# Optimization experiments

Measured on AMD Instinct MI355X. Metric: run time of the kernel, lower is better.

Reference implementation:

```python
import jax, jax.numpy as jnp
import numpy as np

N0, N1, N2 = 200000, 50000, 10000   # source nodes, hop-1 targets, final targets
D, C, DEG = 256, 40, 10


def _sage(x_src, x_tgt, row, col, n_tgt, Wl, Wr, b, reduce):
    # PyG SAGEConv: lin_l(aggr(messages)) + lin_r(x_target); bias on lin_l only
    msg = x_src[row]                                   # [E, D] gather
    if reduce == 'mean':
        s = jax.ops.segment_sum(msg, col, num_segments=n_tgt)
        cnt = jax.ops.segment_sum(jnp.ones((row.shape[0], 1), msg.dtype), col, num_segments=n_tgt)
        agg = s / jnp.maximum(cnt, 1.0)
    else:
        agg = jax.ops.segment_max(msg, col, num_segments=n_tgt)
    return agg @ Wl + b + x_tgt @ Wr


def setup_inputs() -> dict:
    key = jax.random.key(0)
    ks = jax.random.split(key, 16)
    x = jax.random.normal(ks[0], (N0, D), jnp.float32)
    # every target gets exactly DEG sampled neighbors (NeighborSampler-style)
    row0 = jax.random.randint(ks[1], (N1 * DEG,), 0, N0, jnp.int32)
    col0 = jnp.repeat(jnp.arange(N1, dtype=jnp.int32), DEG)
    edge_index0 = jnp.stack([row0, col0])
    row1 = jax.random.randint(ks[2], (N2 * DEG,), 0, N1, jnp.int32)
    col1 = jnp.repeat(jnp.arange(N2, dtype=jnp.int32), DEG)
    edge_index1 = jnp.stack([row1, col1])
    s = 1.0 / np.sqrt(D)
    w = lambda k, shp: jax.random.uniform(k, shp, jnp.float32, -s, s)
    return {
        'x': x, 'edge_index0': edge_index0, 'edge_index1': edge_index1,
        'Wl_m0': w(ks[3], (D, D)), 'Wr_m0': w(ks[4], (D, D)), 'b_m0': jnp.zeros((D,), jnp.float32),
        'Wl_x0': w(ks[5], (D, D)), 'Wr_x0': w(ks[6], (D, D)), 'b_x0': jnp.zeros((D,), jnp.float32),
        'Wl_m1': w(ks[7], (D, D)), 'Wr_m1': w(ks[8], (D, D)), 'b_m1': jnp.zeros((D,), jnp.float32),
        'Wl_x1': w(ks[9], (D, D)), 'Wr_x1': w(ks[10], (D, D)), 'b_x1': jnp.zeros((D,), jnp.float32),
        'W_post': w(ks[11], (2 * D, C)), 'b_post': jnp.zeros((C,), jnp.float32),
    }


def reference(x, edge_index0, edge_index1,
              Wl_m0, Wr_m0, b_m0, Wl_x0, Wr_x0, b_x0,
              Wl_m1, Wr_m1, b_m1, Wl_x1, Wr_x1, b_x1,
              W_post, b_post):
    row0, col0 = edge_index0[0], edge_index0[1]
    row1, col1 = edge_index1[0], edge_index1[1]
    tgt0 = x[:N1]
    h_m = jax.nn.relu(_sage(x, tgt0, row0, col0, N1, Wl_m0, Wr_m0, b_m0, 'mean'))
    h_x = jax.nn.relu(_sage(x, tgt0, row0, col0, N1, Wl_x0, Wr_x0, b_x0, 'max'))
    # NOTE: faithful to source bug: layer-1 target features are the RAW x[:size[1]]
    tgt1 = x[:N2]
    o_m = _sage(h_m, tgt1, row1, col1, N2, Wl_m1, Wr_m1, b_m1, 'mean')
    o_x = _sage(h_x, tgt1, row1, col1, N2, Wl_x1, Wr_x1, b_x1, 'max')
    out = jnp.concatenate([o_m, o_x], axis=-1) @ W_post + b_post
    return jax.nn.log_softmax(out, axis=-1)
```

## Files before the change

kernel.cpp:

```cpp
#include <hip/hip_runtime.h>
#include <hip/hip_bf16.h>
#include <math.h>

#define N0v 200000
#define N1v 50000
#define N2v 10000
#define Dv  256
#define Cv  40
#define DEGv 10

typedef __attribute__((ext_vector_type(8))) short          s16x8;
typedef __attribute__((ext_vector_type(8))) unsigned short u16x8;
typedef __attribute__((ext_vector_type(4))) float          f32x4;

static __device__ __forceinline__ unsigned short f2bf(float f) {
    __hip_bfloat16 h = __float2bfloat16(f);
    return *reinterpret_cast<unsigned short*>(&h);
}
static __device__ __forceinline__ float bf2f(unsigned short u) {
    __hip_bfloat16 h = *reinterpret_cast<__hip_bfloat16*>(&u);
    return __bfloat162float(h);
}

static __device__ __forceinline__ void gload16(const void* g, void* l) {
    __builtin_amdgcn_global_load_lds(
        (const __attribute__((address_space(1))) unsigned int*)g,
        (__attribute__((address_space(3))) unsigned int*)l, 16, 0, 0);
}

__global__ __launch_bounds__(256) void prep_kernel(
    const float* __restrict__ x, unsigned short* __restrict__ xtb,
    const float* __restrict__ Wl0, const float* __restrict__ Wr0,
    const float* __restrict__ Wl1, const float* __restrict__ Wr1,
    const float* __restrict__ Wl2, const float* __restrict__ Wr2,
    const float* __restrict__ Wl3, const float* __restrict__ Wr3,
    unsigned short* __restrict__ WT0, unsigned short* __restrict__ WT1,
    unsigned short* __restrict__ WT2, unsigned short* __restrict__ WT3)
{
    const int b = blockIdx.x;
    const int tid = threadIdx.x;
    if (b < 6250) {
        const int i = (b * 256 + tid) * 8;
        float4 v0 = *(const float4*)(x + i);
        float4 v1 = *(const float4*)(x + i + 4);
        unsigned short o[8] = { f2bf(v0.x), f2bf(v0.y), f2bf(v0.z), f2bf(v0.w),
                                f2bf(v1.x), f2bf(v1.y), f2bf(v1.z), f2bf(v1.w) };
        *(u16x8*)(xtb + i) = *(u16x8*)o;
    } else {
        const int idx = b - 6250;
        const int p = idx >> 8;
        const int n = idx & 255;
        const float* Wl = (p == 0) ? Wl0 : (p == 1) ? Wl1 : (p == 2) ? Wl2 : Wl3;
        const float* Wr = (p == 0) ? Wr0 : (p == 1) ? Wr1 : (p == 2) ? Wr2 : Wr3;
        unsigned short* WT = (p == 0) ? WT0 : (p == 1) ? WT1 : (p == 2) ? WT2 : WT3;
        WT[(size_t)n * 512 + tid]       = f2bf(Wl[(size_t)tid * Dv + n]);
        WT[(size_t)n * 512 + 256 + tid] = f2bf(Wr[(size_t)tid * Dv + n]);
    }
}

__global__ __launch_bounds__(256) void agg0_kernel(
    const float* __restrict__ x, const int* __restrict__ row,
    unsigned short* __restrict__ om, unsigned short* __restrict__ ox)
{
    const int t = blockIdx.x * 4 + (threadIdx.x >> 6);
    const int c = threadIdx.x & 63;
    const int eb = t * DEGv;
    float4 s = make_float4(0.f, 0.f, 0.f, 0.f);
    float4 mx = make_float4(-INFINITY, -INFINITY, -INFINITY, -INFINITY);
#pragma unroll
    for (int k = 0; k < DEGv; ++k) {
        const int r = row[eb + k];
        float4 v = ((const float4*)x)[(size_t)r * 64 + c];
        s.x += v.x; s.y += v.y; s.z += v.z; s.w += v.w;
        mx.x = fmaxf(mx.x, v.x); mx.y = fmaxf(mx.y, v.y);
        mx.z = fmaxf(mx.z, v.z); mx.w = fmaxf(mx.w, v.w);
    }
    const float inv = 1.0f / DEGv;
    unsigned short osum[4] = { f2bf(s.x * inv), f2bf(s.y * inv), f2bf(s.z * inv), f2bf(s.w * inv) };
    unsigned short omax[4] = { f2bf(mx.x), f2bf(mx.y), f2bf(mx.z), f2bf(mx.w) };
    *(uint2*)&om[(size_t)t * Dv + c * 4] = *(uint2*)osum;
    *(uint2*)&ox[(size_t)t * Dv + c * 4] = *(uint2*)omax;
}

__global__ __launch_bounds__(256) void agg1_kernel(
    const unsigned short* __restrict__ hm, const unsigned short* __restrict__ hx,
    const int* __restrict__ row,
    unsigned short* __restrict__ om, unsigned short* __restrict__ ox)
{
    const int t = blockIdx.x * 8 + (threadIdx.x >> 5);
    const int c = threadIdx.x & 31;
    const int eb = t * DEGv;
    float s[8] = {};
    float mx[8] = { -INFINITY, -INFINITY, -INFINITY, -INFINITY,
                    -INFINITY, -INFINITY, -INFINITY, -INFINITY };
#pragma unroll
    for (int k = 0; k < DEGv; ++k) {
        const int r = row[eb + k];
        u16x8 vm = ((const u16x8*)hm)[(size_t)r * 32 + c];
        u16x8 vx = ((const u16x8*)hx)[(size_t)r * 32 + c];
#pragma unroll
        for (int j = 0; j < 8; ++j) {
            s[j]  += bf2f(vm[j]);
            mx[j]  = fmaxf(mx[j], bf2f(vx[j]));
        }
    }
    const float inv = 1.0f / DEGv;
    unsigned short osum[8], omax[8];
#pragma unroll
    for (int j = 0; j < 8; ++j) { osum[j] = f2bf(s[j] * inv); omax[j] = f2bf(mx[j]); }
    *(u16x8*)&om[(size_t)t * Dv + c * 8] = *(u16x8*)osum;
    *(u16x8*)&ox[(size_t)t * Dv + c * 8] = *(u16x8*)omax;
}

template<int RELU, int OUTBF>
__global__ __launch_bounds__(256) void gemm_mfma_kernel(
    const unsigned short* __restrict__ A1a, const unsigned short* __restrict__ A1b,
    const unsigned short* __restrict__ A2,
    const unsigned short* __restrict__ WTa, const unsigned short* __restrict__ WTb,
    const float* __restrict__ biasa, const float* __restrict__ biasb,
    void* outa, void* outb, int M, int ldc, int col_step)
{
    __shared__ unsigned short Asb[128 * 64];
    __shared__ unsigned short Bsb[128 * 64];

    const int z = blockIdx.z;
    const unsigned short* A1 = z ? A1b : A1a;
    const unsigned short* WT = z ? WTb : WTa;
    const float* bias = z ? biasb : biasa;
    void* outp = z ? outb : outa;
    const int col_off = z * col_step;

    const int tid  = threadIdx.x;
    const int lane = tid & 63;
    const int w    = tid >> 6;
    const int wr   = w >> 1, wc = w & 1;
    const int m0   = blockIdx.x * 128, n0 = blockIdx.y * 128;

    const int lrow = lane >> 3;
    const int scol = ((lane & 7) ^ lrow) * 8;

    const unsigned short* pA1[4];
    const unsigned short* pA2[4];
    const unsigned short* pB[4];
    unsigned short* lA[4];
    unsigned short* lB[4];
#pragma unroll
    for (int c = 0; c < 4; ++c) {
        const int r = w * 32 + c * 8 + lrow;
        int gm = m0 + r; if (gm >= M) gm = M - 1;
        pA1[c] = A1 + (size_t)gm * Dv + scol;
        pA2[c] = A2 + (size_t)gm * Dv + scol;
        pB[c]  = WT + (size_t)(n0 + r) * 512 + scol;
        lA[c] = &Asb[(w * 32 + c * 8) * 64];
        lB[c] = &Bsb[(w * 32 + c * 8) * 64];
    }

    const int fr = lane & 15;
    const int f7 = lane & 7;

    f32x4 acc[4][4] = {};

    for (int k0 = 0; k0 < 512; k0 += 64) {
        __syncthreads();
        if (k0 < 256) {
#pragma unroll
            for (int c = 0; c < 4; ++c) gload16(pA1[c] + k0, lA[c]);
        } else {
#pragma unroll
            for (int c = 0; c < 4; ++c) gload16(pA2[c] + (k0 - 256), lA[c]);
        }
#pragma unroll
        for (int c = 0; c < 4; ++c) gload16(pB[c] + k0, lB[c]);
        __syncthreads();

#pragma unroll
        for (int kk = 0; kk < 2; ++kk) {
            const int sl = kk * 4 + (lane >> 4);
            s16x8 af[4], bfr[4];
#pragma unroll
            for (int i = 0; i < 4; ++i) {
                const int ar = wr * 64 + i * 16 + fr;
                af[i]  = *(const s16x8*)&Asb[ar * 64 + ((sl ^ f7) << 3)];
                const int br = wc * 64 + i * 16 + fr;
                bfr[i] = *(const s16x8*)&Bsb[br * 64 + ((sl ^ f7) << 3)];
            }
#pragma unroll
            for (int i = 0; i < 4; ++i)
#pragma unroll
                for (int j = 0; j < 4; ++j)
                    acc[i][j] = __builtin_amdgcn_mfma_f32_16x16x32_bf16(af[i], bfr[j], acc[i][j], 0, 0, 0);
        }
    }

#pragma unroll
    for (int i = 0; i < 4; ++i) {
#pragma unroll
        for (int reg = 0; reg < 4; ++reg) {
            const int gr = m0 + wr * 64 + i * 16 + (lane >> 4) * 4 + reg;
            if (gr < M) {
#pragma unroll
                for (int j = 0; j < 4; ++j) {
                    const int gc = n0 + wc * 64 + j * 16 + fr;
                    float v = acc[i][j][reg] + bias[gc];
                    if (RELU) v = fmaxf(v, 0.0f);
                    if (OUTBF)
                        ((unsigned short*)outp)[(size_t)gr * ldc + col_off + gc] = f2bf(v);
                    else
                        ((float*)outp)[(size_t)gr * ldc + col_off + gc] = v;
                }
            }
        }
    }
}

__global__ __launch_bounds__(64) void post_kernel(
    const unsigned short* __restrict__ ocat, const float* __restrict__ Wp,
    const float* __restrict__ bp, float* __restrict__ out)
{
    __shared__ float srow[2 * Dv];
    __shared__ float slog[Cv];
    __shared__ float s_lse;

    const int t = blockIdx.x;
    const int tid = threadIdx.x;

    for (int i = tid; i < 2 * Dv; i += 64)
        srow[i] = bf2f(ocat[(size_t)t * (2 * Dv) + i]);
    __syncthreads();

    if (tid < Cv) {
        float acc = bp[tid];
#pragma unroll 8
        for (int k = 0; k < 2 * Dv; ++k)
            acc += srow[k] * Wp[(size_t)k * Cv + tid];
        slog[tid] = acc;
    }
    __syncthreads();

    if (tid == 0) {
        float m = slog[0];
        for (int c = 1; c < Cv; ++c) m = fmaxf(m, slog[c]);
        float s = 0.0f;
        for (int c = 0; c < Cv; ++c) s += expf(slog[c] - m);
        s_lse = m + logf(s);
    }
    __syncthreads();

    if (tid < Cv)
        out[(size_t)t * Cv + tid] = slog[tid] - s_lse;
}

extern "C" void kernel_launch(void* const* d_in, const int* in_sizes, int n_in,
                              void* d_out, int out_size, void* d_ws, size_t ws_size,
                              hipStream_t stream)
{
    const float* x      = (const float*)d_in[0];
    const int*   ei0    = (const int*)d_in[1];
    const int*   ei1    = (const int*)d_in[2];
    const float* Wl_m0  = (const float*)d_in[3];
    const float* Wr_m0  = (const float*)d_in[4];
    const float* b_m0   = (const float*)d_in[5];
    const float* Wl_x0  = (const float*)d_in[6];
    const float* Wr_x0  = (const float*)d_in[7];
    const float* b_x0   = (const float*)d_in[8];
    const float* Wl_m1  = (const float*)d_in[9];
    const float* Wr_m1  = (const float*)d_in[10];
    const float* b_m1   = (const float*)d_in[11];
    const float* Wl_x1  = (const float*)d_in[12];
    const float* Wr_x1  = (const float*)d_in[13];
    const float* b_x1   = (const float*)d_in[14];
    const float* W_post = (const float*)d_in[15];
    const float* b_post = (const float*)d_in[16];
    float* out = (float*)d_out;

    const int* row0 = ei0;
    const int* row1 = ei1;

    char* ws = (char*)d_ws;
    const size_t NB = (size_t)N1v * Dv * 2;
    unsigned short* xtb = (unsigned short*)(ws);
    unsigned short* am  = (unsigned short*)(ws + NB);
    unsigned short* ax  = (unsigned short*)(ws + 2 * NB);
    unsigned short* hm  = (unsigned short*)(ws + 3 * NB);
    unsigned short* hx  = (unsigned short*)(ws + 4 * NB);
    unsigned short* a1m = (unsigned short*)(ws + 5 * NB);
    unsigned short* a1x = a1m + (size_t)N2v * Dv;
    unsigned short* ocat = (unsigned short*)(ws + 5 * NB + (size_t)2 * N2v * Dv * 2);
    unsigned short* WT0m = ocat + (size_t)N2v * 2 * Dv;
    unsigned short* WT0x = WT0m + (size_t)256 * 512;
    unsigned short* WT1m = WT0x + (size_t)256 * 512;
    unsigned short* WT1x = WT1m + (size_t)256 * 512;

    const dim3 blk(256);

    prep_kernel<<<6250 + 1024, blk, 0, stream>>>(
        x, xtb,
        Wl_m0, Wr_m0, Wl_x0, Wr_x0, Wl_m1, Wr_m1, Wl_x1, Wr_x1,
        WT0m, WT0x, WT1m, WT1x);
    agg0_kernel<<<N1v / 4, blk, 0, stream>>>(x, row0, am, ax);

    gemm_mfma_kernel<1, 1><<<dim3((N1v + 127) / 128, 2, 2), blk, 0, stream>>>(
        am, ax, xtb, WT0m, WT0x, b_m0, b_x0, hm, hx, N1v, Dv, 0);

    agg1_kernel<<<N2v / 8, blk, 0, stream>>>(hm, hx, row1, a1m, a1x);
    gemm_mfma_kernel<0, 1><<<dim3((N2v + 127) / 128, 2, 2), blk, 0, stream>>>(
        a1m, a1x, xtb, WT1m, WT1x, b_m1, b_x1, ocat, ocat, N2v, 2 * Dv, Dv);

    post_kernel<<<N2v, dim3(64), 0, stream>>>(ocat, W_post, b_post, out);
}
```

Before: 232.7 us.

## Fuse x-to-bf16 conversion into agg0 and tile post kernel over rows

Moves the bf16 conversion of the first N1 rows of x out of the prep kernel and into agg0, so each target row's own features are converted in the same pass that gathers its neighbors. This avoids a separate full pass over x and shrinks the prep launch. The post kernel is restructured so each block handles 32 rows: it stages W_post in shared memory (80 KB), splits the 512-long reduction across 8 thread groups, and combines the partial sums through shared memory before the log-softmax. This replaces a one-row-per-block design that read W_post from global memory for every row, at the cost of heavy shared-memory use and 40-float per-thread accumulators that raise register pressure.

Measured after the change: 224.8 us. 3.4% less time.

```diff
diff --git a/kernel.cpp b/kernel.cpp
--- a/kernel.cpp
+++ b/kernel.cpp
@@ -29,7 +29,6 @@
 }
 
 __global__ __launch_bounds__(256) void prep_kernel(
-    const float* __restrict__ x, unsigned short* __restrict__ xtb,
     const float* __restrict__ Wl0, const float* __restrict__ Wr0,
     const float* __restrict__ Wl1, const float* __restrict__ Wr1,
     const float* __restrict__ Wl2, const float* __restrict__ Wr2,
@@ -37,30 +36,21 @@
     unsigned short* __restrict__ WT0, unsigned short* __restrict__ WT1,
     unsigned short* __restrict__ WT2, unsigned short* __restrict__ WT3)
 {
-    const int b = blockIdx.x;
-    const int tid = threadIdx.x;
-    if (b < 6250) {
-        const int i = (b * 256 + tid) * 8;
-        float4 v0 = *(const float4*)(x + i);
-        float4 v1 = *(const float4*)(x + i + 4);
-        unsigned short o[8] = { f2bf(v0.x), f2bf(v0.y), f2bf(v0.z), f2bf(v0.w),
-                                f2bf(v1.x), f2bf(v1.y), f2bf(v1.z), f2bf(v1.w) };
-        *(u16x8*)(xtb + i) = *(u16x8*)o;
-    } else {
-        const int idx = b - 6250;
-        const int p = idx >> 8;
-        const int n = idx & 255;
-        const float* Wl = (p == 0) ? Wl0 : (p == 1) ? Wl1 : (p == 2) ? Wl2 : Wl3;
-        const float* Wr = (p == 0) ? Wr0 : (p == 1) ? Wr1 : (p == 2) ? Wr2 : Wr3;
-        unsigned short* WT = (p == 0) ? WT0 : (p == 1) ? WT1 : (p == 2) ? WT2 : WT3;
-        WT[(size_t)n * 512 + tid]       = f2bf(Wl[(size_t)tid * Dv + n]);
-        WT[(size_t)n * 512 + 256 + tid] = f2bf(Wr[(size_t)tid * Dv + n]);
-    }
+    const int idx = blockIdx.x;
+    const int p = idx >> 8;
+    const int n = idx & 255;
+    const int k = threadIdx.x;
+    const float* Wl = (p == 0) ? Wl0 : (p == 1) ? Wl1 : (p == 2) ? Wl2 : Wl3;
+    const float* Wr = (p == 0) ? Wr0 : (p == 1) ? Wr1 : (p == 2) ? Wr2 : Wr3;
+    unsigned short* WT = (p == 0) ? WT0 : (p == 1) ? WT1 : (p == 2) ? WT2 : WT3;
+    WT[(size_t)n * 512 + k]       = f2bf(Wl[(size_t)k * Dv + n]);
+    WT[(size_t)n * 512 + 256 + k] = f2bf(Wr[(size_t)k * Dv + n]);
 }
 
 __global__ __launch_bounds__(256) void agg0_kernel(
     const float* __restrict__ x, const int* __restrict__ row,
-    unsigned short* __restrict__ om, unsigned short* __restrict__ ox)
+    unsigned short* __restrict__ om, unsigned short* __restrict__ ox,
+    unsigned short* __restrict__ xtb)
 {
     const int t = blockIdx.x * 4 + (threadIdx.x >> 6);
     const int c = threadIdx.x & 63;
@@ -80,6 +70,10 @@
     unsigned short omax[4] = { f2bf(mx.x), f2bf(mx.y), f2bf(mx.z), f2bf(mx.w) };
     *(uint2*)&om[(size_t)t * Dv + c * 4] = *(uint2*)osum;
     *(uint2*)&ox[(size_t)t * Dv + c * 4] = *(uint2*)omax;
+
+    float4 v = ((const float4*)x)[(size_t)t * 64 + c];
+    unsigned short o[4] = { f2bf(v.x), f2bf(v.y), f2bf(v.z), f2bf(v.w) };
+    *(uint2*)&xtb[(size_t)t * Dv + c * 4] = *(uint2*)o;
 }
 
 __global__ __launch_bounds__(256) void agg1_kernel(
@@ -213,41 +207,80 @@
     }
 }
 
-__global__ __launch_bounds__(64) void post_kernel(
+__global__ __launch_bounds__(256) void post_kernel(
     const unsigned short* __restrict__ ocat, const float* __restrict__ Wp,
-    const float* __restrict__ bp, float* __restrict__ out)
-{
-    __shared__ float srow[2 * Dv];
-    __shared__ float slog[Cv];
-    __shared__ float s_lse;
-
-    const int t = blockIdx.x;
+    const float* __restrict__ bp, float* __restrict__ out, int nrows)
+{
+    __shared__ float sW[512 * 40];
+    __shared__ float sP[7][32][40];
+    __shared__ float sb[Cv];
+
     const int tid = threadIdx.x;
 
-    for (int i = tid; i < 2 * Dv; i += 64)
-        srow[i] = bf2f(ocat[(size_t)t * (2 * Dv) + i]);
+    for (int i = tid; i < 5120; i += 256)
+        ((float4*)sW)[i] = ((const float4*)Wp)[i];
+    if (tid < Cv) sb[tid] = bp[tid];
     __syncthreads();
 
-    if (tid < Cv) {
-        float acc = bp[tid];
-#pragma unroll 8
-        for (int k = 0; k < 2 * Dv; ++k)
-            acc += srow[k] * Wp[(size_t)k * Cv + tid];
-        slog[tid] = acc;
+    const int q = tid >> 5;
+    const int r = tid & 31;
+    const int t = blockIdx.x * 32 + r;
+    const bool valid = (t < nrows);
+
+    float acc[Cv] = {};
+    if (valid) {
+        const unsigned short* prow = ocat + (size_t)t * 512 + q * 64;
+        for (int kk = 0; kk < 64; kk += 8) {
+            u16x8 v = *(const u16x8*)(prow + kk);
+            const float* wbase = &sW[(q * 64 + kk) * Cv];
+#pragma unroll
+            for (int e = 0; e < 8; ++e) {
+                const float xv = bf2f(v[e]);
+                const float* wr_ = wbase + e * Cv;
+#pragma unroll
+                for (int c4 = 0; c4 < Cv; c4 += 4) {
+                    f32x4 wv = *(const f32x4*)(wr_ + c4);
+                    acc[c4 + 0] += xv * wv[0];
+                    acc[c4 + 1] += xv * wv[1];
+                    acc[c4 + 2] += xv * wv[2];
+                    acc[c4 + 3] += xv * wv[3];
+                }
+            }
+        }
+    }
+
+    if (q > 0) {
+#pragma unroll
+        for (int c4 = 0; c4 < Cv; c4 += 4)
+            *(f32x4*)&sP[q - 1][r][c4] = *(f32x4*)&acc[c4];
     }
     __syncthreads();
 
-    if (tid == 0) {
-        float m = slog[0];
-        for (int c = 1; c < Cv; ++c) m = fmaxf(m, slog[c]);
+    if (q == 0 && valid) {
+#pragma unroll
+        for (int p = 0; p < 7; ++p)
+#pragma unroll
+            for (int c4 = 0; c4 < Cv; c4 += 4) {
+                f32x4 pv = *(const f32x4*)&sP[p][r][c4];
+                acc[c4 + 0] += pv[0];
+                acc[c4 + 1] += pv[1];
+                acc[c4 + 2] += pv[2];
+                acc[c4 + 3] += pv[3];
+            }
+        float m = -INFINITY;
+#pragma unroll
+        for (int c = 0; c < Cv; ++c) { acc[c] += sb[c]; m = fmaxf(m, acc[c]); }
         float s = 0.0f;
-        for (int c = 0; c < Cv; ++c) s += expf(slog[c] - m);
-        s_lse = m + logf(s);
-    }
-    __syncthreads();
-
-    if (tid < Cv)
-        out[(size_t)t * Cv + tid] = slog[tid] - s_lse;
+#pragma unroll
+        for (int c = 0; c < Cv; ++c) s += expf(acc[c] - m);
+        const float lse = m + logf(s);
+        float* dst = out + (size_t)t * Cv;
+#pragma unroll
+        for (int c4 = 0; c4 < Cv; c4 += 4) {
+            float o[4] = { acc[c4] - lse, acc[c4 + 1] - lse, acc[c4 + 2] - lse, acc[c4 + 3] - lse };
+            *(float4*)(dst + c4) = *(float4*)o;
+        }
+    }
 }
 
 extern "C" void kernel_launch(void* const* d_in, const int* in_sizes, int n_in,
@@ -293,11 +326,10 @@
 
     const dim3 blk(256);
 
-    prep_kernel<<<6250 + 1024, blk, 0, stream>>>(
-        x, xtb,
+    prep_kernel<<<1024, blk, 0, stream>>>(
         Wl_m0, Wr_m0, Wl_x0, Wr_x0, Wl_m1, Wr_m1, Wl_x1, Wr_x1,
         WT0m, WT0x, WT1m, WT1x);
-    agg0_kernel<<<N1v / 4, blk, 0, stream>>>(x, row0, am, ax);
+    agg0_kernel<<<N1v / 4, blk, 0, stream>>>(x, row0, am, ax, xtb);
 
     gemm_mfma_kernel<1, 1><<<dim3((N1v + 127) / 128, 2, 2), blk, 0, stream>>>(
         am, ax, xtb, WT0m, WT0x, b_m0, b_x0, hm, hx, N1v, Dv, 0);
@@ -306,5 +338,5 @@
     gemm_mfma_kernel<0, 1><<<dim3((N2v + 127) / 128, 2, 2), blk, 0, stream>>>(
         a1m, a1x, xtb, WT1m, WT1x, b_m1, b_x1, ocat, ocat, N2v, 2 * Dv, Dv);
 
-    post_kernel<<<N2v, dim3(64), 0, stream>>>(ocat, W_post, b_post, out);
-}
+    post_kernel<<<(N2v + 31) / 32, blk, 0, stream>>>(ocat, W_post, b_post, out, N2v);
+}
```
